# Optimization experiments

Measured on AMD Instinct MI355X. Metric: run time of the kernel, lower is better.

Reference implementation:

```python
import jax, jax.numpy as jnp
import numpy as np

B, T, DM, DK = 16, 2048, 1024, 128

def setup_inputs() -> dict:
    key = jax.random.key(0)
    k1, k2, k3, k4 = jax.random.split(key, 4)
    x = jax.random.normal(k1, (B, T, DM), dtype=jnp.float32)
    # Linear(dm, dk, bias=False) weights, stored as [dm, dk] for x @ W
    scale = 1.0 / np.sqrt(DM)
    W_q = jax.random.normal(k2, (DM, DK), dtype=jnp.float32) * scale
    W_k = jax.random.normal(k3, (DM, DK), dtype=jnp.float32) * scale
    W_v = jax.random.normal(k4, (DM, DK), dtype=jnp.float32) * scale
    return {"x": x, "W_q": W_q, "W_k": W_k, "W_v": W_v}

def reference(x, W_q, W_k, W_v):
    # q, k, v: [B, T, DK]
    q = jnp.einsum('btd,dk->btk', x, W_q)
    k = jnp.einsum('btd,dk->btk', x, W_k)
    v = jnp.einsum('btd,dk->btk', x, W_v)
    dk = k.shape[-1]
    # scores: [B, T, T], scaled by dk**-0.5
    wei = jnp.einsum('bqk,bsk->bqs', q, k) * (dk ** -0.5)
    # causal mask (tril == 0 -> -inf)
    causal = jnp.tril(jnp.ones((q.shape[1], q.shape[1]), dtype=bool))
    wei = jnp.where(causal, wei, -jnp.inf)
    wei = jax.nn.softmax(wei, axis=-1)
    out = jnp.einsum('bqs,bsk->bqk', wei, v)  # [B, T, DK]
    return out
```

## Files before the change

### kernel.cpp

```cpp
#include <hip/hip_runtime.h>
#include <hip/hip_bf16.h>

#define NB 16
#define NT 2048
#define NDM 1024
#define NDK 128

typedef __bf16 bf16;
typedef bf16 bf16x4 __attribute__((ext_vector_type(4)));
typedef bf16 bf16x8 __attribute__((ext_vector_type(8)));
typedef float f32x4 __attribute__((ext_vector_type(4)));

__device__ inline bf16 to_bf16(float f) {
    __hip_bfloat16 h = __float2bfloat16(f);
    return *reinterpret_cast<bf16*>(&h);
}

__global__ __launch_bounds__(256) void transpose_w_kernel(
        const float* __restrict__ Wq, const float* __restrict__ Wk,
        const float* __restrict__ Wv, bf16* __restrict__ Wt) {
    int idx = blockIdx.x * 256 + threadIdx.x;
    int w = idx >> 17;
    int r = idx & (NDM * NDK - 1);
    int k = r >> 7;
    int n = r & (NDK - 1);
    const float* W = (w == 0) ? Wq : ((w == 1) ? Wk : Wv);
    Wt[(size_t)w * NDK * NDM + (size_t)n * NDM + k] = to_bf16(W[(size_t)k * NDK + n]);
}

__global__ __launch_bounds__(256) void proj_kernel(
        const float* __restrict__ x, const bf16* __restrict__ Wt,
        bf16* __restrict__ qkv, bf16* __restrict__ Vt) {
    __shared__ __align__(16) char smem[128 * 136 * 2];
    bf16 (*As)[40] = reinterpret_cast<bf16(*)[40]>(smem);
    bf16 (*Bs)[40] = reinterpret_cast<bf16(*)[40]>(smem + 10240);
    bf16 (*Tl)[136] = reinterpret_cast<bf16(*)[136]>(smem);

    const int tid = threadIdx.x;
    const int lane = tid & 63;
    const int wave = tid >> 6;
    const int wr = wave >> 1, wc = wave & 1;
    const int r16 = lane & 15, kg = lane >> 4;
    const int mb = blockIdx.x;
    const int w = blockIdx.y;
    const float* xA = x + (size_t)mb * 128 * NDM;
    const bf16* Bt = Wt + (size_t)w * NDK * NDM;

    f32x4 acc[4][4];
#pragma unroll
    for (int m = 0; m < 4; m++)
#pragma unroll
        for (int n = 0; n < 4; n++) acc[m][n] = (f32x4){0.f, 0.f, 0.f, 0.f};

    for (int k0 = 0; k0 < NDM; k0 += 32) {
#pragma unroll
        for (int p = 0; p < 4; p++) {
            int row = p * 32 + (tid >> 3);
            int c4 = (tid & 7) * 4;
            const float4 v = *reinterpret_cast<const float4*>(&xA[(size_t)row * NDM + k0 + c4]);
            bf16x4 bv = { to_bf16(v.x), to_bf16(v.y), to_bf16(v.z), to_bf16(v.w) };
            *reinterpret_cast<bf16x4*>(&As[row][c4]) = bv;
        }
#pragma unroll
        for (int p = 0; p < 2; p++) {
            int idx = (p * 256 + tid) * 8;
            int n = idx >> 5;
            int kk = idx & 31;
            *reinterpret_cast<bf16x8*>(&Bs[n][kk]) =
                *reinterpret_cast<const bf16x8*>(&Bt[(size_t)n * NDM + k0 + kk]);
        }
        __syncthreads();
        bf16x8 af[4], bfr[4];
#pragma unroll
        for (int m = 0; m < 4; m++)
            af[m] = *reinterpret_cast<const bf16x8*>(&As[wr * 64 + m * 16 + r16][kg * 8]);
#pragma unroll
        for (int n = 0; n < 4; n++)
            bfr[n] = *reinterpret_cast<const bf16x8*>(&Bs[wc * 64 + n * 16 + r16][kg * 8]);
#pragma unroll
        for (int m = 0; m < 4; m++)
#pragma unroll
            for (int n = 0; n < 4; n++)
                acc[m][n] = __builtin_amdgcn_mfma_f32_16x16x32_bf16(af[m], bfr[n], acc[m][n], 0, 0, 0);
        __syncthreads();
    }

    if (w < 2) {
        bf16* outw = qkv + (size_t)w * (size_t)(NB * NT) * NDK;
#pragma unroll
        for (int m = 0; m < 4; m++) {
            int rowb = mb * 128 + wr * 64 + m * 16 + kg * 4;
#pragma unroll
            for (int n = 0; n < 4; n++) {
                int col = wc * 64 + n * 16 + r16;
#pragma unroll
                for (int r = 0; r < 4; r++)
                    outw[(size_t)(rowb + r) * NDK + col] = to_bf16(acc[m][n][r]);
            }
        }
    } else {
#pragma unroll
        for (int m = 0; m < 4; m++) {
            int tl = wr * 64 + m * 16 + kg * 4;
#pragma unroll
            for (int n = 0; n < 4; n++) {
                int d = wc * 64 + n * 16 + r16;
                bf16x4 pv = { to_bf16(acc[m][n][0]), to_bf16(acc[m][n][1]),
                              to_bf16(acc[m][n][2]), to_bf16(acc[m][n][3]) };
                *reinterpret_cast<bf16x4*>(&Tl[d][tl]) = pv;
            }
        }
        __syncthreads();
        const int b = mb >> 4;
        const int t0 = (mb & 15) * 128;
        bf16* Vb = Vt + (size_t)b * NDK * NT;
#pragma unroll
        for (int p = 0; p < 8; p++) {
            int idx = p * 256 + tid;
            int d = idx >> 4, c = idx & 15;
            *reinterpret_cast<bf16x8*>(&Vb[(size_t)d * NT + t0 + c * 8]) =
                *reinterpret_cast<const bf16x8*>(&Tl[d][c * 8]);
        }
    }
}

__global__ __launch_bounds__(256) void attn_kernel(
        const bf16* __restrict__ Q, const bf16* __restrict__ K,
        const bf16* __restrict__ Vt, float* __restrict__ out) {
    __shared__ bf16 Ks[2][64][128];
    __shared__ bf16 Vs[2][128][64];
    __shared__ bf16 Ps[4][16][72];
    const int tid = threadIdx.x, lane = tid & 63, wave = tid >> 6;
    const int r16 = lane & 15, kg = lane >> 4;

    const int bid = blockIdx.x;
    const int xcd = bid & 7;
    const int j = bid >> 3;
    const int b = xcd * 2 + (j & 1);
    const int qb = (NT / 64 - 1) - (j >> 1);
    const int q0 = qb * 64;
    const size_t baseB = (size_t)b * NT * NDK;
    const size_t baseVt = (size_t)b * NDK * NT;

    const float scale = 0.08838834764831843f;
    bf16x8 qf[4];
    const int qglob = q0 + wave * 16 + r16;
#pragma unroll
    for (int kc = 0; kc < 4; kc++) {
        bf16x8 raw = *reinterpret_cast<const bf16x8*>(&Q[baseB + (size_t)qglob * NDK + kc * 32 + kg * 8]);
#pragma unroll
        for (int jj = 0; jj < 8; jj++) raw[jj] = to_bf16((float)raw[jj] * scale);
        qf[kc] = raw;
    }

    f32x4 o[8];
#pragma unroll
    for (int n = 0; n < 8; n++) o[n] = (f32x4){0.f, 0.f, 0.f, 0.f};
    float mrun = -INFINITY;
    float lrun = 0.f;

    int krow[4], kcol[4], vrow[4], vcol[4];
#pragma unroll
    for (int i = 0; i < 4; i++) {
        int idx = i * 256 + tid;
        krow[i] = idx >> 4; kcol[i] = idx & 15;
        vrow[i] = idx >> 3; vcol[i] = idx & 7;
    }

    const int nsteps = qb + 1;
    bf16x8 kreg[4], vreg[4];
#pragma unroll
    for (int i = 0; i < 4; i++) {
        kreg[i] = *reinterpret_cast<const bf16x8*>(&K[baseB + (size_t)krow[i] * NDK + kcol[i] * 8]);
        vreg[i] = *reinterpret_cast<const bf16x8*>(&Vt[baseVt + (size_t)vrow[i] * NT + vcol[i] * 8]);
    }
#pragma unroll
    for (int i = 0; i < 4; i++) {
        *reinterpret_cast<bf16x8*>(&Ks[0][krow[i]][(kcol[i] ^ (krow[i] & 7)) * 8]) = kreg[i];
        *reinterpret_cast<bf16x8*>(&Vs[0][vrow[i]][(vcol[i] ^ (vrow[i] & 7)) * 8]) = vreg[i];
    }
    if (nsteps > 1) {
#pragma unroll
        for (int i = 0; i < 4; i++) {
            kreg[i] = *reinterpret_cast<const bf16x8*>(&K[baseB + (size_t)(64 + krow[i]) * NDK + kcol[i] * 8]);
            vreg[i] = *reinterpret_cast<const bf16x8*>(&Vt[baseVt + (size_t)vrow[i] * NT + 64 + vcol[i] * 8]);
        }
    }
    __syncthreads();

    for (int s = 0; s < nsteps; s++) {
        const int cur = s & 1;
        const int kv0 = s * 64;

        f32x4 sfr[4];
#pragma unroll
        for (int n = 0; n < 4; n++) sfr[n] = (f32x4){0.f, 0.f, 0.f, 0.f};
#pragma unroll
        for (int n = 0; n < 4; n++) {
            const int krw = n * 16 + r16;
#pragma unroll
            for (int kc = 0; kc < 4; kc++) {
                bf16x8 kf = *reinterpret_cast<const bf16x8*>(&Ks[cur][krw][((kc * 4 + kg) ^ (krw & 7)) * 8]);
                sfr[n] = __builtin_amdgcn_mfma_f32_16x16x32_bf16(kf, qf[kc], sfr[n], 0, 0, 0);
            }
        }

        if (s == nsteps - 1) {
#pragma unroll
            for (int n = 0; n < 4; n++)
#pragma unroll
                for (int r = 0; r < 4; r++)
                    if (kv0 + n * 16 + kg * 4 + r > qglob) sfr[n][r] = -INFINITY;
        }

        float pm = -INFINITY;
#pragma unroll
        for (int n = 0; n < 4; n++) {
            float t0 = fmaxf(fmaxf(sfr[n][0], sfr[n][1]), fmaxf(sfr[n][2], sfr[n][3]));
            pm = fmaxf(pm, t0);
        }
        pm = fmaxf(pm, __shfl_xor(pm, 16, 64));
        pm = fmaxf(pm, __shfl_xor(pm, 32, 64));

        if (__any(pm > mrun)) {
            float mnew = fmaxf(mrun, pm);
            float corr = __expf(mrun - mnew);
            mrun = mnew;
            lrun *= corr;
            float co[4];
#pragma unroll
            for (int r = 0; r < 4; r++) co[r] = __shfl(corr, kg * 4 + r, 64);
#pragma unroll
            for (int n = 0; n < 8; n++)
#pragma unroll
                for (int r = 0; r < 4; r++) o[n][r] *= co[r];
        }

        float ps = 0.f;
#pragma unroll
        for (int n = 0; n < 4; n++) {
            bf16x4 pw;
#pragma unroll
            for (int r = 0; r < 4; r++) {
                float pv = __expf(sfr[n][r] - mrun);
                ps += pv;
                pw[r] = to_bf16(pv);
            }
            *reinterpret_cast<bf16x4*>(&Ps[wave][r16][n * 16 + kg * 4]) = pw;
        }
        ps += __shfl_xor(ps, 16, 64);
        ps += __shfl_xor(ps, 32, 64);
        lrun += ps;

#pragma unroll
        for (int kc2 = 0; kc2 < 2; kc2++) {
            bf16x8 pf = *reinterpret_cast<const bf16x8*>(&Ps[wave][r16][kc2 * 32 + kg * 8]);
#pragma unroll
            for (int n = 0; n < 8; n++) {
                const int vrw = n * 16 + r16;
                bf16x8 vf = *reinterpret_cast<const bf16x8*>(&Vs[cur][vrw][((kc2 * 4 + kg) ^ (vrw & 7)) * 8]);
                o[n] = __builtin_amdgcn_mfma_f32_16x16x32_bf16(pf, vf, o[n], 0, 0, 0);
            }
        }

        if (s + 1 < nsteps) {
#pragma unroll
            for (int i = 0; i < 4; i++) {
                *reinterpret_cast<bf16x8*>(&Ks[1 - cur][krow[i]][(kcol[i] ^ (krow[i] & 7)) * 8]) = kreg[i];
                *reinterpret_cast<bf16x8*>(&Vs[1 - cur][vrow[i]][(vcol[i] ^ (vrow[i] & 7)) * 8]) = vreg[i];
            }
            if (s + 2 < nsteps) {
                const int kv2 = (s + 2) * 64;
#pragma unroll
                for (int i = 0; i < 4; i++) {
                    kreg[i] = *reinterpret_cast<const bf16x8*>(&K[baseB + (size_t)(kv2 + krow[i]) * NDK + kcol[i] * 8]);
                    vreg[i] = *reinterpret_cast<const bf16x8*>(&Vt[baseVt + (size_t)vrow[i] * NT + kv2 + vcol[i] * 8]);
                }
            }
        }
        __syncthreads();
    }

    float linv = 1.0f / lrun;
    float li[4];
#pragma unroll
    for (int r = 0; r < 4; r++) li[r] = __shfl(linv, kg * 4 + r, 64);
#pragma unroll
    for (int n = 0; n < 8; n++)
#pragma unroll
        for (int r = 0; r < 4; r++) {
            int row = q0 + wave * 16 + kg * 4 + r;
            int col = n * 16 + r16;
            out[baseB + (size_t)row * NDK + col] = o[n][r] * li[r];
        }
}

extern "C" void kernel_launch(void* const* d_in, const int* in_sizes, int n_in,
                              void* d_out, int out_size, void* d_ws, size_t ws_size,
                              hipStream_t stream) {
    const float* x  = (const float*)d_in[0];
    const float* Wq = (const float*)d_in[1];
    const float* Wk = (const float*)d_in[2];
    const float* Wv = (const float*)d_in[3];
    float* out = (float*)d_out;

    char* ws = (char*)d_ws;
    bf16* Wt  = (bf16*)ws;
    bf16* qkv = (bf16*)(ws + (1ull << 20));
    bf16* Vtg = (bf16*)(ws + (26ull << 20));

    transpose_w_kernel<<<(3 * NDM * NDK) / 256, 256, 0, stream>>>(Wq, Wk, Wv, Wt);

    dim3 g1((NB * NT) / 128, 3);
    proj_kernel<<<g1, 256, 0, stream>>>(x, Wt, qkv, Vtg);

    bf16* Qp = qkv;
    bf16* Kp = qkv + (size_t)(NB * NT) * NDK;

    attn_kernel<<<dim3((NT / 64) * NB), 256, 0, stream>>>(Qp, Kp, Vtg, out);
}
```

Baseline: 101.9 us.

## Double-buffer projection GEMM with direct global-to-LDS loads and swizzled layout

Rewrites the projection kernel's main loop to prefetch the next K-tile into a second LDS buffer using global_load_lds, so loading overlaps with MFMA work on the current tile. The x tile is now kept as fp32 in LDS with an XOR swizzle and converted to bf16 at fragment-read time. The W tile is swizzled too to avoid bank conflicts. This costs more LDS (48KB), and the launch bounds now request 3 blocks per SM. The bf16 conversion also moves into the inner loop.

```diff
diff --git a/kernel.cpp b/kernel.cpp
--- a/kernel.cpp
+++ b/kernel.cpp
@@ -14,6 +14,12 @@
 __device__ inline bf16 to_bf16(float f) {
     __hip_bfloat16 h = __float2bfloat16(f);
     return *reinterpret_cast<bf16*>(&h);
+}
+
+__device__ inline void gload_lds16(const void* g, void* l) {
+    __builtin_amdgcn_global_load_lds(
+        (const __attribute__((address_space(1))) unsigned int*)g,
+        (__attribute__((address_space(3))) unsigned int*)l, 16, 0, 0);
 }
 
 __global__ __launch_bounds__(256) void transpose_w_kernel(
@@ -28,13 +34,10 @@
     Wt[(size_t)w * NDK * NDM + (size_t)n * NDM + k] = to_bf16(W[(size_t)k * NDK + n]);
 }
 
-__global__ __launch_bounds__(256) void proj_kernel(
+__global__ __launch_bounds__(256, 3) void proj_kernel(
         const float* __restrict__ x, const bf16* __restrict__ Wt,
         bf16* __restrict__ qkv, bf16* __restrict__ Vt) {
-    __shared__ __align__(16) char smem[128 * 136 * 2];
-    bf16 (*As)[40] = reinterpret_cast<bf16(*)[40]>(smem);
-    bf16 (*Bs)[40] = reinterpret_cast<bf16(*)[40]>(smem + 10240);
-    bf16 (*Tl)[136] = reinterpret_cast<bf16(*)[136]>(smem);
+    __shared__ __align__(16) char smem[49152];
 
     const int tid = threadIdx.x;
     const int lane = tid & 63;
@@ -46,37 +49,65 @@
     const float* xA = x + (size_t)mb * 128 * NDM;
     const bf16* Bt = Wt + (size_t)w * NDK * NDM;
 
+    auto ABUF = [&](int b) -> float* { return (float*)(smem + b * 16384); };
+    auto BBUF = [&](int b) -> bf16*  { return (bf16*)(smem + 32768 + b * 8192); };
+    bf16 (*Tl)[136] = reinterpret_cast<bf16(*)[136]>(smem);
+
+    const int a_row = wave * 8 + (lane >> 3);
+    const int a_c = lane & 7;
+    const int b_row = wave * 16 + (lane >> 2);
+    const int b_c = lane & 3;
+
+    auto stage = [&](int buf, int k0) {
+#pragma unroll
+        for (int p = 0; p < 4; p++) {
+            int row = p * 32 + a_row;
+            int csrc = a_c ^ (row & 7);
+            gload_lds16(xA + (size_t)row * NDM + k0 + csrc * 4,
+                        ABUF(buf) + (p * 256 + wave * 64) * 4);
+        }
+#pragma unroll
+        for (int p = 0; p < 2; p++) {
+            int row = p * 64 + b_row;
+            int csrc = b_c ^ ((row >> 1) & 3);
+            gload_lds16(Bt + (size_t)row * NDM + k0 + csrc * 8,
+                        BBUF(buf) + (p * 256 + wave * 64) * 8);
+        }
+    };
+
     f32x4 acc[4][4];
 #pragma unroll
     for (int m = 0; m < 4; m++)
 #pragma unroll
         for (int n = 0; n < 4; n++) acc[m][n] = (f32x4){0.f, 0.f, 0.f, 0.f};
 
-    for (int k0 = 0; k0 < NDM; k0 += 32) {
-#pragma unroll
-        for (int p = 0; p < 4; p++) {
-            int row = p * 32 + (tid >> 3);
-            int c4 = (tid & 7) * 4;
-            const float4 v = *reinterpret_cast<const float4*>(&xA[(size_t)row * NDM + k0 + c4]);
-            bf16x4 bv = { to_bf16(v.x), to_bf16(v.y), to_bf16(v.z), to_bf16(v.w) };
-            *reinterpret_cast<bf16x4*>(&As[row][c4]) = bv;
-        }
-#pragma unroll
-        for (int p = 0; p < 2; p++) {
-            int idx = (p * 256 + tid) * 8;
-            int n = idx >> 5;
-            int kk = idx & 31;
-            *reinterpret_cast<bf16x8*>(&Bs[n][kk]) =
-                *reinterpret_cast<const bf16x8*>(&Bt[(size_t)n * NDM + k0 + kk]);
-        }
-        __syncthreads();
+    stage(0, 0);
+    __syncthreads();
+
+    for (int kt = 0; kt < NDM / 32; kt++) {
+        const int cur = kt & 1;
+        if (kt + 1 < NDM / 32) stage(1 - cur, (kt + 1) * 32);
+
+        const float* Ac = ABUF(cur);
+        const bf16* Bc = BBUF(cur);
         bf16x8 af[4], bfr[4];
 #pragma unroll
-        for (int m = 0; m < 4; m++)
-            af[m] = *reinterpret_cast<const bf16x8*>(&As[wr * 64 + m * 16 + r16][kg * 8]);
-#pragma unroll
-        for (int n = 0; n < 4; n++)
-            bfr[n] = *reinterpret_cast<const bf16x8*>(&Bs[wc * 64 + n * 16 + r16][kg * 8]);
+        for (int m = 0; m < 4; m++) {
+            int arow = wr * 64 + m * 16 + r16;
+            const float* ap = Ac + arow * 32;
+            float4 lo = *reinterpret_cast<const float4*>(ap + (((kg * 2) ^ (arow & 7)) * 4));
+            float4 hi = *reinterpret_cast<const float4*>(ap + (((kg * 2 + 1) ^ (arow & 7)) * 4));
+            bf16x8 a;
+            a[0] = to_bf16(lo.x); a[1] = to_bf16(lo.y); a[2] = to_bf16(lo.z); a[3] = to_bf16(lo.w);
+            a[4] = to_bf16(hi.x); a[5] = to_bf16(hi.y); a[6] = to_bf16(hi.z); a[7] = to_bf16(hi.w);
+            af[m] = a;
+        }
+#pragma unroll
+        for (int n = 0; n < 4; n++) {
+            int brow = wc * 64 + n * 16 + r16;
+            bfr[n] = *reinterpret_cast<const bf16x8*>(
+                Bc + brow * 32 + ((kg ^ ((brow >> 1) & 3)) * 8));
+        }
 #pragma unroll
         for (int m = 0; m < 4; m++)
 #pragma unroll
```

After: 97.85 us. -3.9%, faster.

## Fuse Q/K/V projections into one block with double-buffered direct-to-LDS loads

Applied to the files above, without the earlier changes.

The projection kernel now computes Q, K and V in one 512-thread block per 128-row tile. Each x tile is read and converted to bf16 once instead of three times. Weight tiles are staged with global_load_lds into double-buffered, XOR-swizzled shared memory, and the next x tile is prefetched into registers while MFMAs run, leaving one barrier per k-step. The cost is more accumulator registers per thread (24 f32x4), 64KB of LDS per block, and a third as many blocks, which may lower occupancy.

```diff
diff --git a/kernel.cpp b/kernel.cpp
--- a/kernel.cpp
+++ b/kernel.cpp
@@ -14,6 +14,12 @@
 __device__ inline bf16 to_bf16(float f) {
     __hip_bfloat16 h = __float2bfloat16(f);
     return *reinterpret_cast<bf16*>(&h);
+}
+
+__device__ inline void gload_lds16(const void* g, void* l) {
+    __builtin_amdgcn_global_load_lds(
+        (const __attribute__((address_space(1))) unsigned int*)g,
+        (__attribute__((address_space(3))) unsigned int*)l, 16, 0, 0);
 }
 
 __global__ __launch_bounds__(256) void transpose_w_kernel(
@@ -28,99 +34,133 @@
     Wt[(size_t)w * NDK * NDM + (size_t)n * NDM + k] = to_bf16(W[(size_t)k * NDK + n]);
 }
 
-__global__ __launch_bounds__(256) void proj_kernel(
+__global__ __launch_bounds__(512) void proj_fused_kernel(
         const float* __restrict__ x, const bf16* __restrict__ Wt,
         bf16* __restrict__ qkv, bf16* __restrict__ Vt) {
-    __shared__ __align__(16) char smem[128 * 136 * 2];
-    bf16 (*As)[40] = reinterpret_cast<bf16(*)[40]>(smem);
-    bf16 (*Bs)[40] = reinterpret_cast<bf16(*)[40]>(smem + 10240);
-    bf16 (*Tl)[136] = reinterpret_cast<bf16(*)[136]>(smem);
-
+    __shared__ __align__(16) char smem[65536];
     const int tid = threadIdx.x;
-    const int lane = tid & 63;
-    const int wave = tid >> 6;
-    const int wr = wave >> 1, wc = wave & 1;
+    const int lane = tid & 63, wave = tid >> 6;
+    const int wr = wave >> 2, wc = wave & 3;
     const int r16 = lane & 15, kg = lane >> 4;
     const int mb = blockIdx.x;
-    const int w = blockIdx.y;
     const float* xA = x + (size_t)mb * 128 * NDM;
-    const bf16* Bt = Wt + (size_t)w * NDK * NDM;
-
-    f32x4 acc[4][4];
-#pragma unroll
-    for (int m = 0; m < 4; m++)
-#pragma unroll
-        for (int n = 0; n < 4; n++) acc[m][n] = (f32x4){0.f, 0.f, 0.f, 0.f};
-
-    for (int k0 = 0; k0 < NDM; k0 += 32) {
-#pragma unroll
-        for (int p = 0; p < 4; p++) {
-            int row = p * 32 + (tid >> 3);
-            int c4 = (tid & 7) * 4;
-            const float4 v = *reinterpret_cast<const float4*>(&xA[(size_t)row * NDM + k0 + c4]);
-            bf16x4 bv = { to_bf16(v.x), to_bf16(v.y), to_bf16(v.z), to_bf16(v.w) };
-            *reinterpret_cast<bf16x4*>(&As[row][c4]) = bv;
-        }
-#pragma unroll
-        for (int p = 0; p < 2; p++) {
-            int idx = (p * 256 + tid) * 8;
-            int n = idx >> 5;
-            int kk = idx & 31;
-            *reinterpret_cast<bf16x8*>(&Bs[n][kk]) =
-                *reinterpret_cast<const bf16x8*>(&Bt[(size_t)n * NDM + k0 + kk]);
-        }
+
+    auto ASB = [&](int b) -> bf16* { return (bf16*)(smem + b * 8192); };
+    auto BSB = [&](int b) -> bf16* { return (bf16*)(smem + 16384 + b * 24576); };
+
+    const int a_row = tid >> 2, a_c = tid & 3;
+    const int a_dst = (a_row * 4 + (a_c ^ ((a_row >> 1) & 3))) * 8;
+    const size_t a_src = (size_t)a_row * NDM + a_c * 8;
+
+    auto loadA = [&](int k0, float4& lo, float4& hi) {
+        lo = *reinterpret_cast<const float4*>(xA + a_src + k0);
+        hi = *reinterpret_cast<const float4*>(xA + a_src + k0 + 4);
+    };
+    auto writeA = [&](int buf, const float4& lo, const float4& hi) {
+        bf16x8 v;
+        v[0] = to_bf16(lo.x); v[1] = to_bf16(lo.y); v[2] = to_bf16(lo.z); v[3] = to_bf16(lo.w);
+        v[4] = to_bf16(hi.x); v[5] = to_bf16(hi.y); v[6] = to_bf16(hi.z); v[7] = to_bf16(hi.w);
+        *reinterpret_cast<bf16x8*>(ASB(buf) + a_dst) = v;
+    };
+    auto stageB = [&](int buf, int k0) {
+#pragma unroll
+        for (int p = 0; p < 3; p++) {
+            int cid = p * 512 + tid;
+            int w = cid >> 9, rem = cid & 511;
+            int row = rem >> 2, c = rem & 3;
+            int cs = c ^ ((row >> 1) & 3);
+            gload_lds16(Wt + (size_t)w * NDK * NDM + (size_t)row * NDM + k0 + cs * 8,
+                        BSB(buf) + (p * 512 + wave * 64) * 8);
+        }
+    };
+
+    f32x4 acc[3][4][2];
+#pragma unroll
+    for (int w = 0; w < 3; w++)
+#pragma unroll
+        for (int m = 0; m < 4; m++)
+#pragma unroll
+            for (int n = 0; n < 2; n++) acc[w][m][n] = (f32x4){0.f, 0.f, 0.f, 0.f};
+
+    {
+        float4 lo, hi;
+        loadA(0, lo, hi);
+        writeA(0, lo, hi);
+        stageB(0, 0);
+    }
+    __syncthreads();
+
+    for (int kt = 0; kt < NDM / 32; kt++) {
+        const int cur = kt & 1;
+        const bool pf = (kt + 1 < NDM / 32);
+        float4 lo, hi;
+        if (pf) {
+            loadA((kt + 1) * 32, lo, hi);
+            stageB(1 - cur, (kt + 1) * 32);
+        }
+
+        bf16x8 af[4];
+#pragma unroll
+        for (int m = 0; m < 4; m++) {
+            int arow = wr * 64 + m * 16 + r16;
+            int ch = kg ^ ((arow >> 1) & 3);
+            af[m] = *reinterpret_cast<const bf16x8*>(ASB(cur) + (arow * 4 + ch) * 8);
+        }
+#pragma unroll
+        for (int w = 0; w < 3; w++) {
+#pragma unroll
+            for (int n = 0; n < 2; n++) {
+                int brow = wc * 32 + n * 16 + r16;
+                int ch = kg ^ ((brow >> 1) & 3);
+                bf16x8 bfw = *reinterpret_cast<const bf16x8*>(
+                    BSB(cur) + ((w * 128 + brow) * 4 + ch) * 8);
+#pragma unroll
+                for (int m = 0; m < 4; m++)
+                    acc[w][m][n] = __builtin_amdgcn_mfma_f32_16x16x32_bf16(af[m], bfw, acc[w][m][n], 0, 0, 0);
+            }
+        }
+
+        if (pf) writeA(1 - cur, lo, hi);
         __syncthreads();
-        bf16x8 af[4], bfr[4];
-#pragma unroll
-        for (int m = 0; m < 4; m++)
-            af[m] = *reinterpret_cast<const bf16x8*>(&As[wr * 64 + m * 16 + r16][kg * 8]);
-#pragma unroll
-        for (int n = 0; n < 4; n++)
-            bfr[n] = *reinterpret_cast<const bf16x8*>(&Bs[wc * 64 + n * 16 + r16][kg * 8]);
-#pragma unroll
-        for (int m = 0; m < 4; m++)
-#pragma unroll
-            for (int n = 0; n < 4; n++)
-                acc[m][n] = __builtin_amdgcn_mfma_f32_16x16x32_bf16(af[m], bfr[n], acc[m][n], 0, 0, 0);
-        __syncthreads();
-    }
-
-    if (w < 2) {
+    }
+
+#pragma unroll
+    for (int w = 0; w < 2; w++) {
         bf16* outw = qkv + (size_t)w * (size_t)(NB * NT) * NDK;
 #pragma unroll
         for (int m = 0; m < 4; m++) {
             int rowb = mb * 128 + wr * 64 + m * 16 + kg * 4;
 #pragma unroll
-            for (int n = 0; n < 4; n++) {
-                int col = wc * 64 + n * 16 + r16;
+            for (int n = 0; n < 2; n++) {
+                int col = wc * 32 + n * 16 + r16;
 #pragma unroll
                 for (int r = 0; r < 4; r++)
-                    outw[(size_t)(rowb + r) * NDK + col] = to_bf16(acc[m][n][r]);
-            }
-        }
-    } else {
-#pragma unroll
-        for (int m = 0; m < 4; m++) {
-            int tl = wr * 64 + m * 16 + kg * 4;
-#pragma unroll
-            for (int n = 0; n < 4; n++) {
-                int d = wc * 64 + n * 16 + r16;
-                bf16x4 pv = { to_bf16(acc[m][n][0]), to_bf16(acc[m][n][1]),
-                              to_bf16(acc[m][n][2]), to_bf16(acc[m][n][3]) };
-                *reinterpret_cast<bf16x4*>(&Tl[d][tl]) = pv;
-            }
-        }
-        __syncthreads();
-        const int b = mb >> 4;
-        const int t0 = (mb & 15) * 128;
-        bf16* Vb = Vt + (size_t)b * NDK * NT;
-#pragma unroll
-        for (int p = 0; p < 8; p++) {
-            int idx = p * 256 + tid;
-            int d = idx >> 4, c = idx & 15;
-            *reinterpret_cast<bf16x8*>(&Vb[(size_t)d * NT + t0 + c * 8]) =
-                *reinterpret_cast<const bf16x8*>(&Tl[d][c * 8]);
-        }
+                    outw[(size_t)(rowb + r) * NDK + col] = to_bf16(acc[w][m][n][r]);
+            }
+        }
+    }
+    bf16 (*Tl)[136] = reinterpret_cast<bf16(*)[136]>(smem);
+#pragma unroll
+    for (int m = 0; m < 4; m++) {
+        int tl = wr * 64 + m * 16 + kg * 4;
+#pragma unroll
+        for (int n = 0; n < 2; n++) {
+            int d = wc * 32 + n * 16 + r16;
+            bf16x4 pv = { to_bf16(acc[2][m][n][0]), to_bf16(acc[2][m][n][1]),
+                          to_bf16(acc[2][m][n][2]), to_bf16(acc[2][m][n][3]) };
+            *reinterpret_cast<bf16x4*>(&Tl[d][tl]) = pv;
+        }
+    }
+    __syncthreads();
+    const int b = mb >> 4;
+    const int t0 = (mb & 15) * 128;
+    bf16* Vb = Vt + (size_t)b * NDK * NT;
+#pragma unroll
+    for (int p = 0; p < 4; p++) {
+        int idx = p * 512 + tid;
+        int d = idx >> 4, c = idx & 15;
+        *reinterpret_cast<bf16x8*>(&Vb[(size_t)d * NT + t0 + c * 8]) =
+            *reinterpret_cast<const bf16x8*>(&Tl[d][c * 8]);
     }
 }
 
@@ -311,8 +351,7 @@
 
     transpose_w_kernel<<<(3 * NDM * NDK) / 256, 256, 0, stream>>>(Wq, Wk, Wv, Wt);
 
-    dim3 g1((NB * NT) / 128, 3);
-    proj_kernel<<<g1, 256, 0, stream>>>(x, Wt, qkv, Vtg);
+    proj_fused_kernel<<<(NB * NT) / 128, 512, 0, stream>>>(x, Wt, qkv, Vtg);
 
     bf16* Qp = qkv;
     bf16* Kp = qkv + (size_t)(NB * NT) * NDK;
```

New measurement: 100.4 us. About the same (-1.4%).

## Fuse Q/K/V projections into one block with larger K tiles and direct-to-LDS loads

Applied to the files above, without the earlier changes.

Each 128-row block now computes all three projections (384 output columns) at once, so x is read and converted to bf16 once instead of three times. The K tile grows to 128 with XOR-swizzled LDS layouts, weights are staged with global_load_lds, and the next x tile is prefetched into registers during the MFMA loop. The block is 512 threads with a 128KB shared buffer and a 4x6 accumulator per wave. This may limit occupancy to one block per CU and raise register pressure.

```diff
diff --git a/kernel.cpp b/kernel.cpp
--- a/kernel.cpp
+++ b/kernel.cpp
@@ -14,6 +14,12 @@
 __device__ inline bf16 to_bf16(float f) {
     __hip_bfloat16 h = __float2bfloat16(f);
     return *reinterpret_cast<bf16*>(&h);
+}
+
+__device__ inline void gload_lds16(const void* g, void* l) {
+    __builtin_amdgcn_global_load_lds(
+        (const __attribute__((address_space(1))) unsigned int*)g,
+        (__attribute__((address_space(3))) unsigned int*)l, 16, 0, 0);
 }
 
 __global__ __launch_bounds__(256) void transpose_w_kernel(
@@ -28,99 +34,123 @@
     Wt[(size_t)w * NDK * NDM + (size_t)n * NDM + k] = to_bf16(W[(size_t)k * NDK + n]);
 }
 
-__global__ __launch_bounds__(256) void proj_kernel(
+__global__ __launch_bounds__(512, 2) void proj_fused_kernel(
         const float* __restrict__ x, const bf16* __restrict__ Wt,
         bf16* __restrict__ qkv, bf16* __restrict__ Vt) {
-    __shared__ __align__(16) char smem[128 * 136 * 2];
-    bf16 (*As)[40] = reinterpret_cast<bf16(*)[40]>(smem);
-    bf16 (*Bs)[40] = reinterpret_cast<bf16(*)[40]>(smem + 10240);
-    bf16 (*Tl)[136] = reinterpret_cast<bf16(*)[136]>(smem);
-
+    __shared__ __align__(16) char smem[131072];
     const int tid = threadIdx.x;
-    const int lane = tid & 63;
-    const int wave = tid >> 6;
-    const int wr = wave >> 1, wc = wave & 1;
+    const int lane = tid & 63, wave = tid >> 6;
+    const int wr = wave >> 2, wc = wave & 3;
     const int r16 = lane & 15, kg = lane >> 4;
     const int mb = blockIdx.x;
-    const int w = blockIdx.y;
     const float* xA = x + (size_t)mb * 128 * NDM;
-    const bf16* Bt = Wt + (size_t)w * NDK * NDM;
-
-    f32x4 acc[4][4];
+
+    bf16* As = (bf16*)smem;
+    bf16* Bs = (bf16*)(smem + 32768);
+
+    const int a_r = tid >> 2;
+    const int a_cb = (tid & 3) * 32;
+
+    float4 areg[8];
+    auto loadA = [&](int kt) {
+        const float* src = xA + (size_t)a_r * NDM + kt * 128 + a_cb;
+#pragma unroll
+        for (int i = 0; i < 8; i++)
+            areg[i] = *reinterpret_cast<const float4*>(src + i * 4);
+    };
+    auto writeA = [&]() {
+#pragma unroll
+        for (int i = 0; i < 4; i++) {
+            int ch = (a_cb >> 3) + i;
+            int chs = ch ^ (a_r & 7);
+            const float4 lo = areg[2 * i], hi = areg[2 * i + 1];
+            bf16x8 v;
+            v[0] = to_bf16(lo.x); v[1] = to_bf16(lo.y); v[2] = to_bf16(lo.z); v[3] = to_bf16(lo.w);
+            v[4] = to_bf16(hi.x); v[5] = to_bf16(hi.y); v[6] = to_bf16(hi.z); v[7] = to_bf16(hi.w);
+            *reinterpret_cast<bf16x8*>(As + a_r * 128 + chs * 8) = v;
+        }
+    };
+    auto stageB = [&](int kt) {
+#pragma unroll
+        for (int p = 0; p < 12; p++) {
+            int D = (p * 8 + wave) * 64 + lane;
+            int brow = D >> 4, bch = D & 15;
+            int sch = bch ^ (brow & 7);
+            gload_lds16(Wt + (size_t)(brow >> 7) * (NDK * NDM)
+                           + (size_t)(brow & 127) * NDM + kt * 128 + sch * 8,
+                        Bs + (size_t)(p * 8 + wave) * 512);
+        }
+    };
+
+    f32x4 acc[4][6];
 #pragma unroll
     for (int m = 0; m < 4; m++)
 #pragma unroll
-        for (int n = 0; n < 4; n++) acc[m][n] = (f32x4){0.f, 0.f, 0.f, 0.f};
-
-    for (int k0 = 0; k0 < NDM; k0 += 32) {
-#pragma unroll
-        for (int p = 0; p < 4; p++) {
-            int row = p * 32 + (tid >> 3);
-            int c4 = (tid & 7) * 4;
-            const float4 v = *reinterpret_cast<const float4*>(&xA[(size_t)row * NDM + k0 + c4]);
-            bf16x4 bv = { to_bf16(v.x), to_bf16(v.y), to_bf16(v.z), to_bf16(v.w) };
-            *reinterpret_cast<bf16x4*>(&As[row][c4]) = bv;
-        }
-#pragma unroll
-        for (int p = 0; p < 2; p++) {
-            int idx = (p * 256 + tid) * 8;
-            int n = idx >> 5;
-            int kk = idx & 31;
-            *reinterpret_cast<bf16x8*>(&Bs[n][kk]) =
-                *reinterpret_cast<const bf16x8*>(&Bt[(size_t)n * NDM + k0 + kk]);
-        }
+        for (int n = 0; n < 6; n++) acc[m][n] = (f32x4){0.f, 0.f, 0.f, 0.f};
+
+    loadA(0);
+    for (int kt = 0; kt < 8; kt++) {
         __syncthreads();
-        bf16x8 af[4], bfr[4];
-#pragma unroll
-        for (int m = 0; m < 4; m++)
-            af[m] = *reinterpret_cast<const bf16x8*>(&As[wr * 64 + m * 16 + r16][kg * 8]);
-#pragma unroll
-        for (int n = 0; n < 4; n++)
-            bfr[n] = *reinterpret_cast<const bf16x8*>(&Bs[wc * 64 + n * 16 + r16][kg * 8]);
-#pragma unroll
-        for (int m = 0; m < 4; m++)
-#pragma unroll
-            for (int n = 0; n < 4; n++)
-                acc[m][n] = __builtin_amdgcn_mfma_f32_16x16x32_bf16(af[m], bfr[n], acc[m][n], 0, 0, 0);
+        writeA();
+        stageB(kt);
         __syncthreads();
-    }
-
-    if (w < 2) {
-        bf16* outw = qkv + (size_t)w * (size_t)(NB * NT) * NDK;
-#pragma unroll
-        for (int m = 0; m < 4; m++) {
-            int rowb = mb * 128 + wr * 64 + m * 16 + kg * 4;
-#pragma unroll
-            for (int n = 0; n < 4; n++) {
-                int col = wc * 64 + n * 16 + r16;
+        if (kt + 1 < 8) loadA(kt + 1);
+
+#pragma unroll
+        for (int kk = 0; kk < 4; kk++) {
+            bf16x8 af[4], bfr[6];
+#pragma unroll
+            for (int m = 0; m < 4; m++) {
+                int arow = wr * 64 + m * 16 + r16;
+                int ch = (kk * 4 + kg) ^ (arow & 7);
+                af[m] = *reinterpret_cast<const bf16x8*>(As + arow * 128 + ch * 8);
+            }
+#pragma unroll
+            for (int nf = 0; nf < 6; nf++) {
+                int brow = wc * 96 + nf * 16 + r16;
+                int ch = (kk * 4 + kg) ^ (brow & 7);
+                bfr[nf] = *reinterpret_cast<const bf16x8*>(Bs + brow * 128 + ch * 8);
+            }
+#pragma unroll
+            for (int m = 0; m < 4; m++)
+#pragma unroll
+                for (int nf = 0; nf < 6; nf++)
+                    acc[m][nf] = __builtin_amdgcn_mfma_f32_16x16x32_bf16(af[m], bfr[nf], acc[m][nf], 0, 0, 0);
+        }
+    }
+
+    __syncthreads();
+    bf16 (*Tl)[136] = reinterpret_cast<bf16(*)[136]>(smem);
+#pragma unroll
+    for (int m = 0; m < 4; m++) {
+        int rowb = mb * 128 + wr * 64 + m * 16 + kg * 4;
+        int tl = wr * 64 + m * 16 + kg * 4;
+#pragma unroll
+        for (int nf = 0; nf < 6; nf++) {
+            int col = wc * 96 + nf * 16 + r16;
+            int w = col >> 7, ncol = col & 127;
+            if (w < 2) {
+                bf16* outw = qkv + (size_t)w * (size_t)(NB * NT) * NDK;
 #pragma unroll
                 for (int r = 0; r < 4; r++)
-                    outw[(size_t)(rowb + r) * NDK + col] = to_bf16(acc[m][n][r]);
-            }
-        }
-    } else {
-#pragma unroll
-        for (int m = 0; m < 4; m++) {
-            int tl = wr * 64 + m * 16 + kg * 4;
-#pragma unroll
-            for (int n = 0; n < 4; n++) {
-                int d = wc * 64 + n * 16 + r16;
-                bf16x4 pv = { to_bf16(acc[m][n][0]), to_bf16(acc[m][n][1]),
-                              to_bf16(acc[m][n][2]), to_bf16(acc[m][n][3]) };
-                *reinterpret_cast<bf16x4*>(&Tl[d][tl]) = pv;
-            }
-        }
-        __syncthreads();
-        const int b = mb >> 4;
-        const int t0 = (mb & 15) * 128;
-        bf16* Vb = Vt + (size_t)b * NDK * NT;
-#pragma unroll
-        for (int p = 0; p < 8; p++) {
-            int idx = p * 256 + tid;
-            int d = idx >> 4, c = idx & 15;
-            *reinterpret_cast<bf16x8*>(&Vb[(size_t)d * NT + t0 + c * 8]) =
-                *reinterpret_cast<const bf16x8*>(&Tl[d][c * 8]);
-        }
+                    outw[(size_t)(rowb + r) * NDK + ncol] = to_bf16(acc[m][nf][r]);
+            } else {
+                bf16x4 pv = { to_bf16(acc[m][nf][0]), to_bf16(acc[m][nf][1]),
+                              to_bf16(acc[m][nf][2]), to_bf16(acc[m][nf][3]) };
+                *reinterpret_cast<bf16x4*>(&Tl[ncol][tl]) = pv;
+            }
+        }
+    }
+    __syncthreads();
+    const int b = mb >> 4;
+    const int t0 = (mb & 15) * 128;
+    bf16* Vb = Vt + (size_t)b * NDK * NT;
+#pragma unroll
+    for (int p = 0; p < 4; p++) {
+        int idx = p * 512 + tid;
+        int d = idx >> 4, c = idx & 15;
+        *reinterpret_cast<bf16x8*>(&Vb[(size_t)d * NT + t0 + c * 8]) =
+            *reinterpret_cast<const bf16x8*>(&Tl[d][c * 8]);
     }
 }
 
@@ -311,8 +341,7 @@
 
     transpose_w_kernel<<<(3 * NDM * NDK) / 256, 256, 0, stream>>>(Wq, Wk, Wv, Wt);
 
-    dim3 g1((NB * NT) / 128, 3);
-    proj_kernel<<<g1, 256, 0, stream>>>(x, Wt, qkv, Vtg);
+    proj_fused_kernel<<<(NB * NT) / 128, 512, 0, stream>>>(x, Wt, qkv, Vtg);
 
     bf16* Qp = qkv;
     bf16* Kp = qkv + (size_t)(NB * NT) * NDK;
```

After: 110.6 us. 1.09x slower.
